# Optimization experiments

Measured on AMD Instinct MI355X. Metric: run time of the kernel, lower is better.

Reference implementation:

```python
import jax, jax.numpy as jnp
import numpy as np
import math

D_MODEL = 1024
NUM_HEADS = 16
HEAD_DIM = D_MODEL // NUM_HEADS


def _xavier(key, out_f, in_f):
    limit = math.sqrt(6.0 / (in_f + out_f))
    return jax.random.uniform(key, (out_f, in_f), jnp.float32, -limit, limit)


def ternarize(w):
    # abs-mean threshold -> {-1, 0, +1}
    abs_mean = jnp.mean(jnp.abs(w))
    return jnp.where(jnp.abs(w) > abs_mean, jnp.sign(w), jnp.zeros_like(w))


def setup_inputs() -> dict:
    key = jax.random.key(0)
    kq, kk, kv, kwq, kwk, kwv, kwo = jax.random.split(key, 7)
    B, S = 2, 2048
    return {
        "query": jax.random.normal(kq, (B, S, D_MODEL), jnp.float32),
        "key": jax.random.normal(kk, (B, S, D_MODEL), jnp.float32),
        "value": jax.random.normal(kv, (B, S, D_MODEL), jnp.float32),
        "w_q": _xavier(kwq, D_MODEL, D_MODEL),
        "w_k": _xavier(kwk, D_MODEL, D_MODEL),
        "w_v": _xavier(kwv, D_MODEL, D_MODEL),
        "w_o": _xavier(kwo, D_MODEL, D_MODEL),
    }


def reference(query, key, value, w_q, w_k, w_v, w_o):
    B, S, _ = query.shape
    # ternary projections (F.linear: x @ W.T)
    q = query @ ternarize(w_q).T
    k = key @ ternarize(w_k).T
    v = value @ ternarize(w_v).T
    # [B, H, S, Dh]
    q = q.reshape(B, S, NUM_HEADS, HEAD_DIM).transpose(0, 2, 1, 3)
    k = k.reshape(B, -1, NUM_HEADS, HEAD_DIM).transpose(0, 2, 1, 3)
    v = v.reshape(B, -1, NUM_HEADS, HEAD_DIM).transpose(0, 2, 1, 3)
    scores = jnp.einsum("bhqd,bhkd->bhqk", q, k) / math.sqrt(HEAD_DIM)
    probs = jax.nn.softmax(scores, axis=-1)
    out = jnp.einsum("bhqk,bhkd->bhqd", probs, v)
    out = out.transpose(0, 2, 1, 3).reshape(B, S, D_MODEL)
    return out @ ternarize(w_o).T
```

## Files before the change

### kernel.cpp

```cpp
#include <hip/hip_runtime.h>
#include <cstdint>
#include <cstddef>

typedef __bf16 bfloat;
typedef __bf16 bf16x8 __attribute__((ext_vector_type(8)));
typedef __bf16 bf16x4 __attribute__((ext_vector_type(4)));
typedef float  f32x4  __attribute__((ext_vector_type(4)));

static constexpr int D  = 1024;
static constexpr int S  = 2048;
static constexpr int B  = 2;
static constexpr int H  = 16;
static constexpr int DH = 64;
static constexpr int M  = B * S;
static constexpr int WMAT_N = 1024 * 1024;

#define MFMA_BF16(a, b, c) __builtin_amdgcn_mfma_f32_16x16x32_bf16((a), (b), (c), 0, 0, 0)

__device__ __forceinline__ void gl_lds16(const void* g, void* l) {
  __builtin_amdgcn_global_load_lds(
      (const __attribute__((address_space(1))) void*)g,
      (__attribute__((address_space(3))) void*)l, 16, 0, 0);
}

__global__ void prep_kernel(const float* __restrict__ w0, const float* __restrict__ w1,
                            const float* __restrict__ w2, const float* __restrict__ w3,
                            double* __restrict__ sums) {
  const int y = blockIdx.y;
  const float* w = (y == 0) ? w0 : (y == 1) ? w1 : (y == 2) ? w2 : w3;
  const float4* w4 = (const float4*)w;
  double s = 0.0;
  for (int i = blockIdx.x * blockDim.x + threadIdx.x; i < (WMAT_N / 4);
       i += gridDim.x * blockDim.x) {
    float4 v = w4[i];
    s += (double)fabsf(v.x) + (double)fabsf(v.y) + (double)fabsf(v.z) + (double)fabsf(v.w);
  }
  for (int off = 1; off < 64; off <<= 1) s += __shfl_xor(s, off, 64);
  __shared__ double ps[4];
  if ((threadIdx.x & 63) == 0) ps[threadIdx.x >> 6] = s;
  __syncthreads();
  if (threadIdx.x == 0) atomicAdd(&sums[y], ps[0] + ps[1] + ps[2] + ps[3]);
}

__global__ void tern_kernel(const float* __restrict__ w0, const float* __restrict__ w1,
                            const float* __restrict__ w2, const float* __restrict__ w3,
                            bfloat* __restrict__ o0, bfloat* __restrict__ o1,
                            bfloat* __restrict__ o2, bfloat* __restrict__ o3,
                            const double* __restrict__ sums) {
  int z = blockIdx.y;
  const float* w = (z == 0) ? w0 : (z == 1) ? w1 : (z == 2) ? w2 : w3;
  bfloat* o = (z == 0) ? o0 : (z == 1) ? o1 : (z == 2) ? o2 : o3;
  double thr = sums[z] * (1.0 / (double)WMAT_N);
  const float4* w4 = (const float4*)w;
  for (int i = blockIdx.x * blockDim.x + threadIdx.x; i < (WMAT_N / 4);
       i += gridDim.x * blockDim.x) {
    float4 v = w4[i];
    bf16x4 r;
    r[0] = (bfloat)(((double)fabsf(v.x) > thr) ? (v.x > 0.f ? 1.f : -1.f) : 0.f);
    r[1] = (bfloat)(((double)fabsf(v.y) > thr) ? (v.y > 0.f ? 1.f : -1.f) : 0.f);
    r[2] = (bfloat)(((double)fabsf(v.z) > thr) ? (v.z > 0.f ? 1.f : -1.f) : 0.f);
    r[3] = (bfloat)(((double)fabsf(v.w) > thr) ? (v.w > 0.f ? 1.f : -1.f) : 0.f);
    *(bf16x4*)&o[(size_t)i * 4] = r;
  }
}

__global__ __launch_bounds__(256) void qkv_gemm(
    const float* __restrict__ xq, const float* __restrict__ xk,
    const float* __restrict__ xv, const bfloat* __restrict__ wqt,
    const bfloat* __restrict__ wkt, const bfloat* __restrict__ wvt,
    bfloat* __restrict__ qmh, bfloat* __restrict__ qml,
    bfloat* __restrict__ kmh, bfloat* __restrict__ kml, bfloat* __restrict__ vtr) {
  constexpr int K = D;
  constexpr int N = D;
  __shared__ __align__(16) bfloat As0[128 * 64];
  __shared__ __align__(16) bfloat As1[128 * 64];
  __shared__ __align__(16) bfloat Ws[128 * 64];

  const int bid = blockIdx.x;
  const int xcd = bid & 7;
  const int i6 = bid >> 3;
  const int slice = xcd * 12 + (i6 >> 3);
  const int bx = i6 & 7;
  const int z = slice >> 5;
  const int by = slice & 31;

  const float* Af;
  const bfloat* Wm;
  bfloat *Oh = nullptr, *Ol = nullptr;
  float scale = 1.f;
  bool split;
  if (z == 0) {
    Af = xq; Wm = wqt; Oh = qmh; Ol = qml;
    scale = 0.18033688f;
    split = true;
  } else if (z == 1) {
    Af = xk; Wm = wkt; Oh = kmh; Ol = kml; split = true;
  } else {
    Af = xv; Wm = wvt; split = false;
  }

  const int t = threadIdx.x;
  const int w = t >> 6, lane = t & 63;
  const int quad = lane >> 4, l16 = lane & 15;
  const int wm = w >> 1, wn = w & 1;
  const int m0 = by * 128, n0 = bx * 128;

  f32x4 acc[4][4] = {};

  const int srr = lane >> 3;
  const int spc = lane & 7;
  const int cl8 = (spc ^ srr) * 8;

  const float* aSrc[4];
#pragma unroll
  for (int g = 0; g < 4; g++)
    aSrc[g] = Af + (size_t)(m0 + w * 32 + g * 8 + srr) * K + cl8;

  float4 fa[4][2];
#pragma unroll
  for (int g = 0; g < 4; g++) {
    fa[g][0] = *(const float4*)(aSrc[g]);
    fa[g][1] = *(const float4*)(aSrc[g] + 4);
  }

  for (int kk = 0; kk < K; kk += 64) {
#pragma unroll
    for (int g = 0; g < 4; g++) {
      int rb = w * 32 + g * 8;
      gl_lds16(Wm + (size_t)(n0 + rb + srr) * K + kk + cl8, Ws + rb * 64);
    }
#pragma unroll
    for (int g = 0; g < 4; g++) {
      int row = w * 32 + g * 8 + srr;
      float f[8] = {fa[g][0].x, fa[g][0].y, fa[g][0].z, fa[g][0].w,
                    fa[g][1].x, fa[g][1].y, fa[g][1].z, fa[g][1].w};
      bf16x8 hh;
#pragma unroll
      for (int j = 0; j < 8; j++) hh[j] = (bfloat)f[j];
      const int da = row * 64 + spc * 8;
      *(bf16x8*)&As0[da] = hh;
      if (split) {
        bf16x8 ll;
#pragma unroll
        for (int j = 0; j < 8; j++) ll[j] = (bfloat)(f[j] - (float)hh[j]);
        *(bf16x8*)&As1[da] = ll;
      }
    }
    asm volatile("s_waitcnt vmcnt(0) lgkmcnt(0)" ::: "memory");
    __builtin_amdgcn_s_barrier();
    asm volatile("" ::: "memory");

    if (kk + 64 < K) {
#pragma unroll
      for (int g = 0; g < 4; g++) {
        fa[g][0] = *(const float4*)(aSrc[g] + kk + 64);
        fa[g][1] = *(const float4*)(aSrc[g] + kk + 64 + 4);
      }
    }

#pragma unroll
    for (int kidx = 0; kidx < 2; kidx++) {
      bf16x8 bfrag[4], afrag[4];
#pragma unroll
      for (int nt = 0; nt < 4; nt++) {
        int r = wn * 64 + nt * 16 + l16;
        bfrag[nt] = *(const bf16x8*)&Ws[r * 64 + (((kidx * 4 + quad) ^ (r & 7)) * 8)];
      }
#pragma unroll
      for (int mt = 0; mt < 4; mt++) {
        int r = wm * 64 + mt * 16 + l16;
        afrag[mt] = *(const bf16x8*)&As0[r * 64 + (((kidx * 4 + quad) ^ (r & 7)) * 8)];
      }
#pragma unroll
      for (int mt = 0; mt < 4; mt++)
#pragma unroll
        for (int nt = 0; nt < 4; nt++)
          acc[mt][nt] = MFMA_BF16(afrag[mt], bfrag[nt], acc[mt][nt]);
      if (split) {
#pragma unroll
        for (int mt = 0; mt < 4; mt++) {
          int r = wm * 64 + mt * 16 + l16;
          afrag[mt] = *(const bf16x8*)&As1[r * 64 + (((kidx * 4 + quad) ^ (r & 7)) * 8)];
        }
#pragma unroll
        for (int mt = 0; mt < 4; mt++)
#pragma unroll
          for (int nt = 0; nt < 4; nt++)
            acc[mt][nt] = MFMA_BF16(afrag[mt], bfrag[nt], acc[mt][nt]);
      }
    }
    asm volatile("" ::: "memory");
    __builtin_amdgcn_s_barrier();
    asm volatile("" ::: "memory");
  }

#pragma unroll
  for (int mt = 0; mt < 4; mt++) {
#pragma unroll
    for (int nt = 0; nt < 4; nt++) {
      const int row = m0 + wm * 64 + mt * 16 + quad * 4;
      const int col = n0 + wn * 64 + nt * 16 + l16;
      if (split) {
#pragma unroll
        for (int rg = 0; rg < 4; rg++) {
          float vv = acc[mt][nt][rg] * scale;
          size_t idx = (size_t)(row + rg) * N + col;
          bfloat hh = (bfloat)vv;
          Oh[idx] = hh;
          Ol[idx] = (bfloat)(vv - (float)hh);
        }
      } else {
        int bb = row >> 11, s = row & (S - 1);
        int kk6 = s & 63;
        int pos = (kk6 & 3) | (((kk6 >> 4) & 1) << 2) | (((kk6 >> 2) & 3) << 3) |
                  ((kk6 >> 5) << 5);
        int sp = (s & ~63) | pos;
        bf16x4 pk;
#pragma unroll
        for (int rg = 0; rg < 4; rg++) pk[rg] = (bfloat)acc[mt][nt][rg];
        *(bf16x4*)&vtr[(size_t)bb * D * S + (size_t)col * S + sp] = pk;
      }
    }
  }
}

__global__ __launch_bounds__(256, 4) void gemm_wo(const bfloat* __restrict__ A,
                                                  const bfloat* __restrict__ Wm,
                                                  float* __restrict__ Cf) {
  constexpr int K = D;
  constexpr int N = D;
  __shared__ __align__(16) bfloat As[64 * 128];
  __shared__ __align__(16) bfloat Ws[64 * 128];

  const int bid = blockIdx.x;
  const int xcd = bid & 7;
  const int i7 = bid >> 3;
  const int by = xcd * 8 + (i7 >> 4);
  const int bx = i7 & 15;

  const int t = threadIdx.x;
  const int w = t >> 6, lane = t & 63;
  const int quad = lane >> 4, l16 = lane & 15;
  const int wm = w >> 1, wn = w & 1;
  const int m0 = by * 64, n0 = bx * 64;

  f32x4 acc[2][2] = {};

  const int srr = lane >> 4;
  const int spc = lane & 15;

  for (int kk = 0; kk < K; kk += 128) {
#pragma unroll
    for (int g = 0; g < 4; g++) {
      int row = w * 16 + g * 4 + srr;
      int cl = spc ^ (row & 7);
      int lo = (w * 16 + g * 4) * 128;
      gl_lds16(A + (size_t)(m0 + row) * K + kk + cl * 8, As + lo);
      gl_lds16(Wm + (size_t)(n0 + row) * K + kk + cl * 8, Ws + lo);
    }
    __syncthreads();

#pragma unroll
    for (int kidx = 0; kidx < 4; kidx++) {
      bf16x8 af[2], bfr[2];
#pragma unroll
      for (int i = 0; i < 2; i++) {
        int ar = wm * 32 + i * 16 + l16;
        af[i] = *(const bf16x8*)&As[ar * 128 + (((kidx * 4 + quad) ^ (ar & 7)) * 8)];
        int br = wn * 32 + i * 16 + l16;
        bfr[i] = *(const bf16x8*)&Ws[br * 128 + (((kidx * 4 + quad) ^ (br & 7)) * 8)];
      }
#pragma unroll
      for (int mt = 0; mt < 2; mt++)
#pragma unroll
        for (int nt = 0; nt < 2; nt++)
          acc[mt][nt] = MFMA_BF16(af[mt], bfr[nt], acc[mt][nt]);
    }
    __syncthreads();
  }

#pragma unroll
  for (int mt = 0; mt < 2; mt++) {
#pragma unroll
    for (int nt = 0; nt < 2; nt++) {
      const int row = m0 + wm * 32 + mt * 16 + quad * 4;
      const int col = n0 + wn * 32 + nt * 16 + l16;
#pragma unroll
      for (int rg = 0; rg < 4; rg++) Cf[(size_t)(row + rg) * N + col] = acc[mt][nt][rg];
    }
  }
}

__global__ __launch_bounds__(512) void flash_kernel(
    const bfloat* __restrict__ qh, const bfloat* __restrict__ ql,
    const bfloat* __restrict__ kh, const bfloat* __restrict__ kl,
    const bfloat* __restrict__ vt, bfloat* __restrict__ outp) {
  __shared__ __align__(16) bfloat SM[20480];

  const int tid = threadIdx.x;
  const int w = tid >> 6, lane = tid & 63;
  const int quad = lane >> 4, l16 = lane & 15;

  const int blk = blockIdx.x;
  const int xcd = blk & 7, slot = blk >> 3;
  const int g = xcd * 4 + (slot >> 4);
  const int h = g & 15, b = g >> 4;
  const int q0 = (slot & 15) * 128;

  const size_t base = (size_t)b * S * D + (size_t)h * DH;
  const size_t vbase = (size_t)b * D * S + (size_t)h * DH * S;

  const int ssr = lane >> 3;
  const int spc = lane & 7;
  const int c8 = (spc ^ ssr) * 8;
  const int stKV = w * 512;

  const bfloat* pKh = kh + base + (size_t)(w * 8 + ssr) * D + c8;
  const bfloat* pKl = kl + base + (size_t)(w * 8 + ssr) * D + c8;
  const bfloat* pV = vt + vbase + (size_t)(w * 8 + ssr) * S + c8;

  bf16x8 ones;
#pragma unroll
  for (int j = 0; j < 8; j++) ones[j] = (bfloat)1.f;

  {
    const bfloat* pQh = qh + base + (size_t)(q0 + w * 16 + ssr) * D + c8;
    const bfloat* pQl = ql + base + (size_t)(q0 + w * 16 + ssr) * D + c8;
    gl_lds16(pQh, SM + w * 1024);
    gl_lds16(pQh + 8 * D, SM + w * 1024 + 512);
    gl_lds16(pQl, SM + 8192 + w * 1024);
    gl_lds16(pQl + 8 * D, SM + 8192 + w * 1024 + 512);
  }
  asm volatile("s_waitcnt vmcnt(0)" ::: "memory");
  __builtin_amdgcn_s_barrier();
  asm volatile("" ::: "memory");

  const int fo0 = l16 * 64 + ((quad ^ (l16 & 7)) * 8);
  const int fo4 = fo0 ^ 32;
  const int fq = w * 1024;

  bf16x8 qhf0 = *(const bf16x8*)&SM[fq + fo0];
  bf16x8 qhf1 = *(const bf16x8*)&SM[fq + fo4];
  bf16x8 qlf0 = *(const bf16x8*)&SM[8192 + fq + fo0];
  bf16x8 qlf1 = *(const bf16x8*)&SM[8192 + fq + fo4];
  asm volatile("s_waitcnt lgkmcnt(0)" ::: "memory");
  __builtin_amdgcn_s_barrier();
  asm volatile("" ::: "memory");

  gl_lds16(pKh, SM + 0 + stKV);
  gl_lds16(pKl, SM + 4096 + stKV);
  pKh += 64 * D;
  pKl += 64 * D;
  asm volatile("s_waitcnt vmcnt(0)" ::: "memory");

  f32x4 Oa[4] = {};
  f32x4 La = {};
  float m_i = -3.0e38f;
  constexpr int NT = S / 64;

  for (int t = 0; t < NT; ++t) {
    __builtin_amdgcn_s_barrier();
    asm volatile("" ::: "memory");
    const int cur = (t & 1) * 8192;
    const int nxt = 8192 - cur;

    gl_lds16(pV, SM + 16384 + stKV);
    pV += 64;
    if (t < NT - 1) {
      gl_lds16(pKh, SM + nxt + stKV);
      gl_lds16(pKl, SM + nxt + 4096 + stKV);
      pKh += 64 * D;
      pKl += 64 * D;
    }

    f32x4 sf[4];
    __builtin_amdgcn_s_setprio(1);
#pragma unroll
    for (int mt = 0; mt < 4; mt++) {
      f32x4 a = {};
      bf16x8 bh0 = *(const bf16x8*)&SM[cur + fo0 + mt * 1024];
      bf16x8 bl0 = *(const bf16x8*)&SM[cur + 4096 + fo0 + mt * 1024];
      bf16x8 bh1 = *(const bf16x8*)&SM[cur + fo4 + mt * 1024];
      bf16x8 bl1 = *(const bf16x8*)&SM[cur + 4096 + fo4 + mt * 1024];
      a = MFMA_BF16(bh0, qhf0, a);
      a = MFMA_BF16(bl0, qhf0, a);
      a = MFMA_BF16(bh0, qlf0, a);
      a = MFMA_BF16(bh1, qhf1, a);
      a = MFMA_BF16(bl1, qhf1, a);
      a = MFMA_BF16(bh1, qlf1, a);
      sf[mt] = a;
    }
    __builtin_amdgcn_s_setprio(0);

    float t0 = fmaxf(fmaxf(sf[0][0], sf[0][1]), fmaxf(sf[0][2], sf[0][3]));
    float t1 = fmaxf(fmaxf(sf[1][0], sf[1][1]), fmaxf(sf[1][2], sf[1][3]));
    float t2 = fmaxf(fmaxf(sf[2][0], sf[2][1]), fmaxf(sf[2][2], sf[2][3]));
    float t3 = fmaxf(fmaxf(sf[3][0], sf[3][1]), fmaxf(sf[3][2], sf[3][3]));
    float mm = fmaxf(fmaxf(t0, t1), fmaxf(t2, t3));
    mm = fmaxf(mm, __shfl_xor(mm, 16, 64));
    mm = fmaxf(mm, __shfl_xor(mm, 32, 64));
    if (__ballot(mm > m_i + 8.0f)) {
      float mnew = fmaxf(m_i, mm);
      float alpha = exp2f(m_i - mnew);
      m_i = mnew;
#pragma unroll
      for (int mt = 0; mt < 4; mt++) Oa[mt] *= alpha;
      La *= alpha;
    }
#pragma unroll
    for (int mt = 0; mt < 4; mt++)
#pragma unroll
      for (int rg = 0; rg < 4; rg++) sf[mt][rg] = exp2f(sf[mt][rg] - m_i);

    if (t < NT - 1)
      asm volatile("s_waitcnt vmcnt(2)" ::: "memory");
    else
      asm volatile("s_waitcnt vmcnt(0)" ::: "memory");
    __builtin_amdgcn_s_barrier();
    asm volatile("" ::: "memory");

    __builtin_amdgcn_s_setprio(1);
#pragma unroll
    for (int kp = 0; kp < 2; kp++) {
      bf16x8 pb8;
#pragma unroll
      for (int rg = 0; rg < 4; rg++) {
        pb8[rg] = (bfloat)sf[2 * kp][rg];
        pb8[4 + rg] = (bfloat)sf[2 * kp + 1][rg];
      }
      La = MFMA_BF16(ones, pb8, La);
      const int fv = kp ? fo4 : fo0;
#pragma unroll
      for (int mt = 0; mt < 4; mt++) {
        bf16x8 va = *(const bf16x8*)&SM[16384 + fv + mt * 1024];
        Oa[mt] = MFMA_BF16(va, pb8, Oa[mt]);
      }
    }
    __builtin_amdgcn_s_setprio(0);
    asm volatile("s_waitcnt vmcnt(0)" ::: "memory");
  }

  float inv = 1.0f / La[0];
  const int qrow = q0 + w * 16 + l16;
#pragma unroll
  for (int mt = 0; mt < 4; mt++) {
    bf16x4 ov;
#pragma unroll
    for (int rg = 0; rg < 4; rg++) ov[rg] = (bfloat)(Oa[mt][rg] * inv);
    *(bf16x4*)&outp[base + (size_t)qrow * D + mt * 16 + quad * 4] = ov;
  }
}

extern "C" void kernel_launch(void* const* d_in, const int* in_sizes, int n_in,
                              void* d_out, int out_size, void* d_ws, size_t ws_size,
                              hipStream_t stream) {
  const float* q_in = (const float*)d_in[0];
  const float* k_in = (const float*)d_in[1];
  const float* v_in = (const float*)d_in[2];
  const float* wq = (const float*)d_in[3];
  const float* wk = (const float*)d_in[4];
  const float* wv = (const float*)d_in[5];
  const float* wo = (const float*)d_in[6];
  float* outp = (float*)d_out;
  char* ws = (char*)d_ws;

  constexpr size_t WBYTES = (size_t)WMAT_N * 2;
  constexpr size_t XBYTES = (size_t)M * D * 2;
  size_t off = 0;
  double* sums = (double*)(ws + off); off += 256;
  bfloat* wqt = (bfloat*)(ws + off); off += WBYTES;
  bfloat* wkt = (bfloat*)(ws + off); off += WBYTES;
  bfloat* wvt = (bfloat*)(ws + off); off += WBYTES;
  bfloat* wot = (bfloat*)(ws + off); off += WBYTES;
  bfloat* qmh = (bfloat*)(ws + off); off += XBYTES;
  bfloat* qml = (bfloat*)(ws + off); off += XBYTES;
  bfloat* kmh = (bfloat*)(ws + off); off += XBYTES;
  bfloat* kml = (bfloat*)(ws + off); off += XBYTES;
  bfloat* vtr = (bfloat*)(ws + off); off += XBYTES;
  bfloat* attn = (bfloat*)(ws + off); off += XBYTES;

  hipMemsetAsync(sums, 0, 4 * sizeof(double), stream);
  prep_kernel<<<dim3(256, 4), 256, 0, stream>>>(wq, wk, wv, wo, sums);
  tern_kernel<<<dim3(128, 4), 256, 0, stream>>>(wq, wk, wv, wo, wqt, wkt, wvt, wot, sums);
  qkv_gemm<<<768, 256, 0, stream>>>(
      q_in, k_in, v_in, wqt, wkt, wvt, qmh, qml, kmh, kml, vtr);
  flash_kernel<<<512, 512, 0, stream>>>(qmh, qml, kmh, kml, vtr, attn);
  gemm_wo<<<1024, 256, 0, stream>>>(attn, wot, outp);
}
```

Measured before the change: 271.6 us.

## Fuse ternarization kernels with grid barrier; register-stage weight tiles in QKV GEMM

```diff
diff --git a/kernel.cpp b/kernel.cpp
--- a/kernel.cpp
+++ b/kernel.cpp
@@ -23,44 +23,52 @@
       (__attribute__((address_space(3))) void*)l, 16, 0, 0);
 }
 
-__global__ void prep_kernel(const float* __restrict__ w0, const float* __restrict__ w1,
-                            const float* __restrict__ w2, const float* __restrict__ w3,
-                            double* __restrict__ sums) {
-  const int y = blockIdx.y;
-  const float* w = (y == 0) ? w0 : (y == 1) ? w1 : (y == 2) ? w2 : w3;
-  const float4* w4 = (const float4*)w;
-  double s = 0.0;
-  for (int i = blockIdx.x * blockDim.x + threadIdx.x; i < (WMAT_N / 4);
-       i += gridDim.x * blockDim.x) {
-    float4 v = w4[i];
-    s += (double)fabsf(v.x) + (double)fabsf(v.y) + (double)fabsf(v.z) + (double)fabsf(v.w);
-  }
-  for (int off = 1; off < 64; off <<= 1) s += __shfl_xor(s, off, 64);
-  __shared__ double ps[4];
-  if ((threadIdx.x & 63) == 0) ps[threadIdx.x >> 6] = s;
+__global__ void tern_fused(const float* __restrict__ w0, const float* __restrict__ w1,
+                           const float* __restrict__ w2, const float* __restrict__ w3,
+                           bfloat* __restrict__ o0, bfloat* __restrict__ o1,
+                           bfloat* __restrict__ o2, bfloat* __restrict__ o3,
+                           double* __restrict__ sums, unsigned int* __restrict__ cnt) {
+  const int tid = threadIdx.x;
+  const int nb = gridDim.x;
+  __shared__ double thr_s[4];
+
+#pragma unroll
+  for (int z = 0; z < 4; z++) {
+    const float* w = (z == 0) ? w0 : (z == 1) ? w1 : (z == 2) ? w2 : w3;
+    const float4* w4 = (const float4*)w;
+    double s = 0.0;
+    for (int i = blockIdx.x * blockDim.x + tid; i < (WMAT_N / 4); i += nb * blockDim.x) {
+      float4 v = w4[i];
+      s += (double)fabsf(v.x) + (double)fabsf(v.y) + (double)fabsf(v.z) + (double)fabsf(v.w);
+    }
+    for (int off = 1; off < 64; off <<= 1) s += __shfl_xor(s, off, 64);
+    if ((tid & 63) == 0) atomicAdd(&sums[z], s);
+  }
+  __threadfence();
   __syncthreads();
-  if (threadIdx.x == 0) atomicAdd(&sums[y], ps[0] + ps[1] + ps[2] + ps[3]);
-}
-
-__global__ void tern_kernel(const float* __restrict__ w0, const float* __restrict__ w1,
-                            const float* __restrict__ w2, const float* __restrict__ w3,
-                            bfloat* __restrict__ o0, bfloat* __restrict__ o1,
-                            bfloat* __restrict__ o2, bfloat* __restrict__ o3,
-                            const double* __restrict__ sums) {
-  int z = blockIdx.y;
-  const float* w = (z == 0) ? w0 : (z == 1) ? w1 : (z == 2) ? w2 : w3;
-  bfloat* o = (z == 0) ? o0 : (z == 1) ? o1 : (z == 2) ? o2 : o3;
-  double thr = sums[z] * (1.0 / (double)WMAT_N);
-  const float4* w4 = (const float4*)w;
-  for (int i = blockIdx.x * blockDim.x + threadIdx.x; i < (WMAT_N / 4);
-       i += gridDim.x * blockDim.x) {
-    float4 v = w4[i];
-    bf16x4 r;
-    r[0] = (bfloat)(((double)fabsf(v.x) > thr) ? (v.x > 0.f ? 1.f : -1.f) : 0.f);
-    r[1] = (bfloat)(((double)fabsf(v.y) > thr) ? (v.y > 0.f ? 1.f : -1.f) : 0.f);
-    r[2] = (bfloat)(((double)fabsf(v.z) > thr) ? (v.z > 0.f ? 1.f : -1.f) : 0.f);
-    r[3] = (bfloat)(((double)fabsf(v.w) > thr) ? (v.w > 0.f ? 1.f : -1.f) : 0.f);
-    *(bf16x4*)&o[(size_t)i * 4] = r;
+  if (tid == 0) {
+    atomicAdd(cnt, 1u);
+    while (atomicAdd(cnt, 0u) < (unsigned)nb) { __builtin_amdgcn_s_sleep(8); }
+  }
+  __syncthreads();
+  if (tid < 4) thr_s[tid] = atomicAdd(&sums[tid], 0.0) * (1.0 / (double)WMAT_N);
+  __syncthreads();
+
+#pragma unroll
+  for (int z = 0; z < 4; z++) {
+    const float* w = (z == 0) ? w0 : (z == 1) ? w1 : (z == 2) ? w2 : w3;
+    bfloat* o = (z == 0) ? o0 : (z == 1) ? o1 : (z == 2) ? o2 : o3;
+    const double thr = thr_s[z];
+    const float4* w4 = (const float4*)w;
+    for (int i = blockIdx.x * blockDim.x + tid; i < (WMAT_N / 4); i += nb * blockDim.x) {
+      float4 v = w4[i];
+      bf16x4 r;
+      r[0] = (bfloat)(((double)fabsf(v.x) > thr) ? (v.x > 0.f ? 1.f : -1.f) : 0.f);
+      r[1] = (bfloat)(((double)fabsf(v.y) > thr) ? (v.y > 0.f ? 1.f : -1.f) : 0.f);
+      r[2] = (bfloat)(((double)fabsf(v.z) > thr) ? (v.z > 0.f ? 1.f : -1.f) : 0.f);
+      r[3] = (bfloat)(((double)fabsf(v.w) > thr) ? (v.w > 0.f ? 1.f : -1.f) : 0.f);
+      *(bf16x4*)&o[(size_t)i * 4] = r;
+    }
   }
 }
 
@@ -112,32 +120,33 @@
   const int cl8 = (spc ^ srr) * 8;
 
   const float* aSrc[4];
-#pragma unroll
-  for (int g = 0; g < 4; g++)
+  const bfloat* wSrc[4];
+#pragma unroll
+  for (int g = 0; g < 4; g++) {
     aSrc[g] = Af + (size_t)(m0 + w * 32 + g * 8 + srr) * K + cl8;
+    wSrc[g] = Wm + (size_t)(n0 + w * 32 + g * 8 + srr) * K + cl8;
+  }
 
   float4 fa[4][2];
+  bf16x8 fw[4];
 #pragma unroll
   for (int g = 0; g < 4; g++) {
     fa[g][0] = *(const float4*)(aSrc[g]);
     fa[g][1] = *(const float4*)(aSrc[g] + 4);
+    fw[g] = *(const bf16x8*)(wSrc[g]);
   }
 
   for (int kk = 0; kk < K; kk += 64) {
-#pragma unroll
-    for (int g = 0; g < 4; g++) {
-      int rb = w * 32 + g * 8;
-      gl_lds16(Wm + (size_t)(n0 + rb + srr) * K + kk + cl8, Ws + rb * 64);
-    }
 #pragma unroll
     for (int g = 0; g < 4; g++) {
       int row = w * 32 + g * 8 + srr;
+      const int da = row * 64 + spc * 8;
+      *(bf16x8*)&Ws[da] = fw[g];
       float f[8] = {fa[g][0].x, fa[g][0].y, fa[g][0].z, fa[g][0].w,
                     fa[g][1].x, fa[g][1].y, fa[g][1].z, fa[g][1].w};
       bf16x8 hh;
 #pragma unroll
       for (int j = 0; j < 8; j++) hh[j] = (bfloat)f[j];
-      const int da = row * 64 + spc * 8;
       *(bf16x8*)&As0[da] = hh;
       if (split) {
         bf16x8 ll;
@@ -146,7 +155,7 @@
         *(bf16x8*)&As1[da] = ll;
       }
     }
-    asm volatile("s_waitcnt vmcnt(0) lgkmcnt(0)" ::: "memory");
+    asm volatile("s_waitcnt lgkmcnt(0)" ::: "memory");
     __builtin_amdgcn_s_barrier();
     asm volatile("" ::: "memory");
 
@@ -155,6 +164,7 @@
       for (int g = 0; g < 4; g++) {
         fa[g][0] = *(const float4*)(aSrc[g] + kk + 64);
         fa[g][1] = *(const float4*)(aSrc[g] + kk + 64 + 4);
+        fw[g] = *(const bf16x8*)(wSrc[g] + kk + 64);
       }
     }
 
@@ -467,7 +477,9 @@
   constexpr size_t WBYTES = (size_t)WMAT_N * 2;
   constexpr size_t XBYTES = (size_t)M * D * 2;
   size_t off = 0;
-  double* sums = (double*)(ws + off); off += 256;
+  double* sums = (double*)(ws + off);
+  unsigned int* cnt = (unsigned int*)(ws + 32);
+  off += 256;
   bfloat* wqt = (bfloat*)(ws + off); off += WBYTES;
   bfloat* wkt = (bfloat*)(ws + off); off += WBYTES;
   bfloat* wvt = (bfloat*)(ws + off); off += WBYTES;
@@ -479,9 +491,8 @@
   bfloat* vtr = (bfloat*)(ws + off); off += XBYTES;
   bfloat* attn = (bfloat*)(ws + off); off += XBYTES;
 
-  hipMemsetAsync(sums, 0, 4 * sizeof(double), stream);
-  prep_kernel<<<dim3(256, 4), 256, 0, stream>>>(wq, wk, wv, wo, sums);
-  tern_kernel<<<dim3(128, 4), 256, 0, stream>>>(wq, wk, wv, wo, wqt, wkt, wvt, wot, sums);
+  hipMemsetAsync(sums, 0, 256, stream);
+  tern_fused<<<256, 256, 0, stream>>>(wq, wk, wv, wo, wqt, wkt, wvt, wot, sums, cnt);
   qkv_gemm<<<768, 256, 0, stream>>>(
       q_in, k_in, v_in, wqt, wkt, wvt, qmh, qml, kmh, kml, vtr);
   flash_kernel<<<512, 512, 0, stream>>>(qmh, qml, kmh, kml, vtr, attn);
```

Result: slower. 324.3 us (+19.4%).
